# Optimization experiments

Hardware: AMD Instinct MI355X
Metric: run time of the kernel (lower is better)

The kernel has to match this reference:

```python
import jax, jax.numpy as jnp
import numpy as np

NT, C, B, N, H, E = 32768, 128, 64, 512, 4, 524288  # total nodes, channels, graphs, nodes/graph, heads, edges
DH = C // H
EPS = 1e-5


def batchnorm(x, g, b):
    # BatchNorm1d over the node dimension (training-mode batch statistics)
    m = x.mean(axis=0)
    v = x.var(axis=0)
    return (x - m) * jax.lax.rsqrt(v + EPS) * g + b


def setup_inputs() -> dict:
    key = jax.random.key(0)
    ks = jax.random.split(key, 8)
    s = 1.0 / np.sqrt(C)
    return dict(
        x=jax.random.normal(ks[0], (NT, C), jnp.float32),
        edge_index=jax.random.randint(ks[1], (2, E), 0, NT, dtype=jnp.int32),
        Wc=jax.random.normal(ks[2], (C, C), jnp.float32) * s,
        bc=jnp.zeros((C,), jnp.float32),
        in_proj_w=jax.random.normal(ks[3], (3 * C, C), jnp.float32) * s,
        in_proj_b=jnp.zeros((3 * C,), jnp.float32),
        out_proj_w=jax.random.normal(ks[4], (C, C), jnp.float32) * s,
        out_proj_b=jnp.zeros((C,), jnp.float32),
        gn1=jnp.ones((C,), jnp.float32), bn1=jnp.zeros((C,), jnp.float32),
        gn2=jnp.ones((C,), jnp.float32), bn2=jnp.zeros((C,), jnp.float32),
        gn3=jnp.ones((C,), jnp.float32), bn3=jnp.zeros((C,), jnp.float32),
        Wm1=jax.random.normal(ks[5], (2 * C, C), jnp.float32) * s,
        bm1=jnp.zeros((2 * C,), jnp.float32),
        Wm2=jax.random.normal(ks[6], (C, 2 * C), jnp.float32) / np.sqrt(2 * C),
        bm2=jnp.zeros((C,), jnp.float32),
    )


def reference(x, edge_index, Wc, bc, in_proj_w, in_proj_b, out_proj_w, out_proj_b,
              gn1, bn1, gn2, bn2, gn3, bn3, Wm1, bm1, Wm2, bm2):
    # --- local branch: mean-aggregation message passing + linear + residual + BN ---
    src, dst = edge_index[0], edge_index[1]
    agg = jax.ops.segment_sum(x[src], dst, num_segments=NT)            # [NT, C]
    cnt = jax.ops.segment_sum(jnp.ones((E, 1), x.dtype), dst, num_segments=NT)
    agg = agg / jnp.maximum(cnt, 1.0)
    h_local = agg @ Wc.T + bc + x                                       # dropout p=0 -> no-op
    h_local = batchnorm(h_local, gn1, bn1)

    # --- global branch: to_dense_batch (equal-size graphs -> reshape) + MHA ---
    hd = x.reshape(B, N, C)
    qkv = hd @ in_proj_w.T + in_proj_b                                  # [B, N, 3C]
    q, k, v = jnp.split(qkv, 3, axis=-1)
    q = q.reshape(B, N, H, DH).transpose(0, 2, 1, 3)                    # [B, H, N, DH]
    k = k.reshape(B, N, H, DH).transpose(0, 2, 1, 3)
    v = v.reshape(B, N, H, DH).transpose(0, 2, 1, 3)
    scores = jnp.einsum('bhqd,bhkd->bhqk', q, k) / np.sqrt(DH)          # [B, H, N, N]
    attn = jax.nn.softmax(scores, axis=-1)
    o = jnp.einsum('bhqk,bhkd->bhqd', attn, v)                          # [B, H, N, DH]
    o = o.transpose(0, 2, 1, 3).reshape(B, N, C)
    h_attn = (o @ out_proj_w.T + out_proj_b).reshape(NT, C) + x
    h_attn = batchnorm(h_attn, gn2, bn2)

    # --- combine + MLP + final norm ---
    out = h_local + h_attn
    out = out + (jax.nn.relu(out @ Wm1.T + bm1) @ Wm2.T + bm2)
    return batchnorm(out, gn3, bn3)
```

## Files before the change

kernel.cpp:

```cpp
#include <hip/hip_runtime.h>
#include <cstddef>

#define NT    32768
#define CCH   128
#define BB    64
#define NNODE 512
#define NHEAD 4
#define DHEAD 32
#define EE    524288
#define EPS   1e-5f
#define MAXDEG 96
#define SRCPAD 100
#define CURPAD 16
#define SSLOT  8

typedef unsigned short u16;
typedef unsigned int   u32;
typedef __attribute__((ext_vector_type(8))) short short8;
typedef __attribute__((ext_vector_type(4))) short short4v;
typedef __attribute__((ext_vector_type(4))) float f32x4;

__device__ __forceinline__ float b2f(u32 w) { return __uint_as_float(w << 16); }
__device__ __forceinline__ u16 f2b(float f) {
    u32 u = __float_as_uint(f);
    u += 0x7FFF + ((u >> 16) & 1);
    return (u16)(u >> 16);
}

__global__ __launch_bounds__(256) void prep_kernel(const float* __restrict__ x,
                                                   const float* __restrict__ Wc,
                                                   const float* __restrict__ Wqkv,
                                                   const float* __restrict__ Wo,
                                                   const float* __restrict__ Wm1,
                                                   const float* __restrict__ Wm2,
                                                   u16* __restrict__ xb,
                                                   u16* __restrict__ Wcb,
                                                   u16* __restrict__ Wqkvb,
                                                   u16* __restrict__ Wob,
                                                   u16* __restrict__ Wm1b,
                                                   u16* __restrict__ Wm2b,
                                                   const int* __restrict__ ei,
                                                   int* __restrict__ cursor,
                                                   int* __restrict__ bucket) {
    if (blockIdx.x >= 2120) {
        int e = (blockIdx.x - 2120) * 256 + threadIdx.x;
        int src = ei[e];
        int dst = ei[EE + e];
        int pos = atomicAdd(cursor + dst * CURPAD, 1);
        if (pos < MAXDEG) bucket[dst * MAXDEG + pos] = src;
        return;
    }
    int r = blockIdx.x * 256 + threadIdx.x;
    const float* src; u16* dst;
    if (r < 524288) { src = x; dst = xb; }
    else if ((r -= 524288) < 2048) { src = Wc; dst = Wcb; }
    else if ((r -= 2048) < 6144) { src = Wqkv; dst = Wqkvb; }
    else if ((r -= 6144) < 2048) { src = Wo; dst = Wob; }
    else if ((r -= 2048) < 4096) { src = Wm1; dst = Wm1b; }
    else { r -= 4096; src = Wm2; dst = Wm2b; }
    size_t base = (size_t)r * 8;
    float4 a = *(const float4*)(src + base);
    float4 b = *(const float4*)(src + base + 4);
    uint4 u;
    u.x = (u32)f2b(a.x) | ((u32)f2b(a.y) << 16);
    u.y = (u32)f2b(a.z) | ((u32)f2b(a.w) << 16);
    u.z = (u32)f2b(b.x) | ((u32)f2b(b.y) << 16);
    u.w = (u32)f2b(b.z) | ((u32)f2b(b.w) << 16);
    *(uint4*)(dst + base) = u;
}

__global__ __launch_bounds__(256) void aggregate(const int* __restrict__ bucket,
                                                 const int* __restrict__ cursor,
                                                 const u16* __restrict__ xb,
                                                 u16* __restrict__ agg) {
    __shared__ int srcs[16][SRCPAD];
    int ln = threadIdx.x >> 4;
    int c8 = threadIdx.x & 15;
    int n = blockIdx.x * 16 + ln;
    int d = min(cursor[n * CURPAD], MAXDEG);
    for (int j = c8; j < d; j += 16) srcs[ln][j] = bucket[n * MAXDEG + j];
    __syncthreads();
    float s0 = 0.f, s1 = 0.f, s2 = 0.f, s3 = 0.f;
    float s4 = 0.f, s5 = 0.f, s6 = 0.f, s7 = 0.f;
    const u16* xp = xb + c8 * 8;
    int j = 0;
    for (; j + 2 <= d; j += 2) {
        uint4 w0 = *(const uint4*)(xp + (size_t)srcs[ln][j] * CCH);
        uint4 w1 = *(const uint4*)(xp + (size_t)srcs[ln][j + 1] * CCH);
        s0 += b2f(w0.x & 0xffffu) + b2f(w1.x & 0xffffu);
        s1 += b2f(w0.x >> 16)     + b2f(w1.x >> 16);
        s2 += b2f(w0.y & 0xffffu) + b2f(w1.y & 0xffffu);
        s3 += b2f(w0.y >> 16)     + b2f(w1.y >> 16);
        s4 += b2f(w0.z & 0xffffu) + b2f(w1.z & 0xffffu);
        s5 += b2f(w0.z >> 16)     + b2f(w1.z >> 16);
        s6 += b2f(w0.w & 0xffffu) + b2f(w1.w & 0xffffu);
        s7 += b2f(w0.w >> 16)     + b2f(w1.w >> 16);
    }
    if (j < d) {
        uint4 w0 = *(const uint4*)(xp + (size_t)srcs[ln][j] * CCH);
        s0 += b2f(w0.x & 0xffffu);
        s1 += b2f(w0.x >> 16);
        s2 += b2f(w0.y & 0xffffu);
        s3 += b2f(w0.y >> 16);
        s4 += b2f(w0.z & 0xffffu);
        s5 += b2f(w0.z >> 16);
        s6 += b2f(w0.w & 0xffffu);
        s7 += b2f(w0.w >> 16);
    }
    float inv = 1.0f / fmaxf((float)d, 1.0f);
    uint4 out;
    out.x = (u32)f2b(s0 * inv) | ((u32)f2b(s1 * inv) << 16);
    out.y = (u32)f2b(s2 * inv) | ((u32)f2b(s3 * inv) << 16);
    out.z = (u32)f2b(s4 * inv) | ((u32)f2b(s5 * inv) << 16);
    out.w = (u32)f2b(s6 * inv) | ((u32)f2b(s7 * inv) << 16);
    *(uint4*)(agg + (size_t)n * CCH + c8 * 8) = out;
}

struct GemmSmem {
    u16 As[128 * 32];
    u16 Bs[128 * 32];
    u16 Cs[4][16 * 72];
    float csum[128];
    float csq[128];
};

template <bool RELU, int RESID, bool STATS>
__device__ __forceinline__ void gemm_body(GemmSmem& sm,
                                          const u16* __restrict__ A,
                                          const u16* __restrict__ W,
                                          const float* __restrict__ bias,
                                          const u16* __restrict__ residb,
                                          u16* __restrict__ outb, int ostride,
                                          float* __restrict__ sum, float* __restrict__ sumsq,
                                          int slotbase, int m0, int K) {
    int tid = threadIdx.x;
    int lane = tid & 63, wave = tid >> 6;
    int wm = (wave & 1) * 64, wn = (wave >> 1) * 64;
    int l15 = lane & 15, l4 = lane >> 4;

    if (STATS) {
        if (tid < 128) { sm.csum[tid] = 0.f; sm.csq[tid] = 0.f; }
    }

    f32x4 zero = {0.f, 0.f, 0.f, 0.f};
    f32x4 acc[4][4];
#pragma unroll
    for (int i = 0; i < 4; ++i)
#pragma unroll
        for (int j = 0; j < 4; ++j) acc[i][j] = zero;

    int srow = tid >> 2;
    int scol = (tid & 3) * 8;

    int kIter = K >> 5;
    uint4 a0 = *(const uint4*)(A + (size_t)(m0 + srow) * K + scol);
    uint4 a1 = *(const uint4*)(A + (size_t)(m0 + srow + 64) * K + scol);
    uint4 b0 = *(const uint4*)(W + (size_t)srow * K + scol);
    uint4 b1 = *(const uint4*)(W + (size_t)(srow + 64) * K + scol);
    for (int ki = 0; ki < kIter; ++ki) {
        if (ki) __syncthreads();
        *(uint4*)&sm.As[srow * 32 + scol] = a0;
        *(uint4*)&sm.As[(srow + 64) * 32 + scol] = a1;
        *(uint4*)&sm.Bs[srow * 32 + scol] = b0;
        *(uint4*)&sm.Bs[(srow + 64) * 32 + scol] = b1;
        if (ki + 1 < kIter) {
            int k0 = (ki + 1) * 32;
            a0 = *(const uint4*)(A + (size_t)(m0 + srow) * K + k0 + scol);
            a1 = *(const uint4*)(A + (size_t)(m0 + srow + 64) * K + k0 + scol);
            b0 = *(const uint4*)(W + (size_t)srow * K + k0 + scol);
            b1 = *(const uint4*)(W + (size_t)(srow + 64) * K + k0 + scol);
        }
        __syncthreads();
        short8 af[4], bf[4];
#pragma unroll
        for (int t = 0; t < 4; ++t) {
            af[t] = *(const short8*)&sm.As[(wm + t * 16 + l15) * 32 + l4 * 8];
            bf[t] = *(const short8*)&sm.Bs[(wn + t * 16 + l15) * 32 + l4 * 8];
        }
#pragma unroll
        for (int mt = 0; mt < 4; ++mt)
#pragma unroll
            for (int nt = 0; nt < 4; ++nt)
                acc[mt][nt] = __builtin_amdgcn_mfma_f32_16x16x32_bf16(af[mt], bf[nt], acc[mt][nt], 0, 0, 0);
    }

    float ps[4] = {0.f, 0.f, 0.f, 0.f};
    float pq[4] = {0.f, 0.f, 0.f, 0.f};
    int rl = lane >> 3;
    int cg = lane & 7;
#pragma unroll
    for (int mt = 0; mt < 4; ++mt) {
#pragma unroll
        for (int nt = 0; nt < 4; ++nt) {
            int lcol = wn + nt * 16 + l15;
            float bs = bias[lcol];
#pragma unroll
            for (int r = 0; r < 4; ++r) {
                int row = m0 + wm + mt * 16 + l4 * 4 + r;
                float v = acc[mt][nt][r] + bs;
                if (RESID == 2) v += b2f(residb[(size_t)row * 128 + lcol]);
                if (RELU) v = fmaxf(v, 0.0f);
                sm.Cs[wave][(l4 * 4 + r) * 72 + nt * 16 + l15] = f2b(v);
                if (STATS) { ps[nt] += v; pq[nt] += v * v; }
            }
        }
#pragma unroll
        for (int p = 0; p < 2; ++p) {
            int lrow = p * 8 + rl;
            uint4 wv = *(const uint4*)&sm.Cs[wave][lrow * 72 + cg * 8];
            int grow = m0 + wm + mt * 16 + lrow;
            *(uint4*)(outb + (size_t)grow * ostride + wn + cg * 8) = wv;
        }
    }
    if (STATS) {
#pragma unroll
        for (int nt = 0; nt < 4; ++nt) {
            atomicAdd(&sm.csum[wn + nt * 16 + l15], ps[nt]);
            atomicAdd(&sm.csq[wn + nt * 16 + l15], pq[nt]);
        }
        __syncthreads();
        if (tid < 128) {
            atomicAdd(sum + slotbase + tid, sm.csum[tid]);
            atomicAdd(sumsq + slotbase + tid, sm.csq[tid]);
        }
    }
}

__global__ __launch_bounds__(256) void gemm_wc_qkv(const u16* __restrict__ aggb,
                                                   const u16* __restrict__ Wcb,
                                                   const float* __restrict__ bc,
                                                   const u16* __restrict__ xb,
                                                   u16* __restrict__ hlocb,
                                                   float* __restrict__ sum1,
                                                   float* __restrict__ sq1,
                                                   const u16* __restrict__ Wqkvb,
                                                   const float* __restrict__ bqkv,
                                                   u16* __restrict__ qkvb) {
    __shared__ GemmSmem sm;
    int y = blockIdx.y;
    int m0 = blockIdx.x * 128;
    if (y == 0) {
        gemm_body<false, 2, true>(sm, aggb, Wcb, bc, xb, hlocb, 128, sum1, sq1,
                                  (blockIdx.x & (SSLOT - 1)) << 7, m0, 128);
    } else {
        gemm_body<false, 0, false>(sm, xb, Wqkvb + (size_t)(y - 1) * 16384,
                                   bqkv + (y - 1) * 128, nullptr,
                                   qkvb + (y - 1) * 128, 384, nullptr, nullptr, 0, m0, 128);
    }
}

__global__ __launch_bounds__(256) void gemm_wo(const u16* __restrict__ ob,
                                               const u16* __restrict__ Wob,
                                               const float* __restrict__ bo,
                                               const u16* __restrict__ xb,
                                               u16* __restrict__ t2b,
                                               float* __restrict__ sum2, float* __restrict__ sq2) {
    __shared__ GemmSmem sm;
    gemm_body<false, 2, true>(sm, ob, Wob, bo, xb, t2b, 128, sum2, sq2,
                              (blockIdx.x & (SSLOT - 1)) << 7, blockIdx.x * 128, 128);
}

__global__ __launch_bounds__(256) void gemm_mlp2(const u16* __restrict__ hidb,
                                                 const u16* __restrict__ Wm2b,
                                                 const float* __restrict__ bm2,
                                                 const u16* __restrict__ shb,
                                                 u16* __restrict__ out2b,
                                                 float* __restrict__ sum3, float* __restrict__ sq3) {
    __shared__ GemmSmem sm;
    gemm_body<false, 2, true>(sm, hidb, Wm2b, bm2, shb, out2b, 128, sum3, sq3,
                              (blockIdx.x & (SSLOT - 1)) << 7, blockIdx.x * 128, 256);
}

__global__ __launch_bounds__(256) void gemm_m1c(const u16* __restrict__ hlocb,
                                                const u16* __restrict__ t2b,
                                                const float* __restrict__ sum1,
                                                const float* __restrict__ sq1,
                                                const float* __restrict__ g1,
                                                const float* __restrict__ bt1,
                                                const float* __restrict__ sum2,
                                                const float* __restrict__ sq2,
                                                const float* __restrict__ g2,
                                                const float* __restrict__ bt2,
                                                u16* __restrict__ shb,
                                                const u16* __restrict__ Wm1b,
                                                const float* __restrict__ bm1,
                                                u16* __restrict__ hidb) {
    __shared__ u16 As[128 * 32];
    __shared__ u16 Bs[128 * 32];
    __shared__ u16 Cs[4][16 * 72];
    __shared__ float AF1[128], BF1[128], AF2[128], BF2[128];
    int tid = threadIdx.x;
    {
        int c = tid & 127;
        const float* sm = (tid < 128) ? sum1 : sum2;
        const float* sq = (tid < 128) ? sq1 : sq2;
        const float* g  = (tid < 128) ? g1 : g2;
        const float* bt = (tid < 128) ? bt1 : bt2;
        float s = 0.f, q = 0.f;
#pragma unroll
        for (int sl = 0; sl < SSLOT; ++sl) { s += sm[sl * 128 + c]; q += sq[sl * 128 + c]; }
        float m = s * (1.0f / NT);
        float v = q * (1.0f / NT) - m * m;
        float a = g[c] * rsqrtf(v + EPS);
        if (tid < 128) { AF1[c] = a; BF1[c] = bt[c] - m * a; }
        else           { AF2[c] = a; BF2[c] = bt[c] - m * a; }
    }
    int m0 = blockIdx.x * 128, n0 = blockIdx.y * 128;
    int lane = tid & 63, wave = tid >> 6;
    int wm = (wave & 1) * 64, wn = (wave >> 1) * 64;
    int l15 = lane & 15, l4 = lane >> 4;

    f32x4 zero = {0.f, 0.f, 0.f, 0.f};
    f32x4 acc[4][4];
#pragma unroll
    for (int i = 0; i < 4; ++i)
#pragma unroll
        for (int j = 0; j < 4; ++j) acc[i][j] = zero;

    int srow = tid >> 2;
    int scol = (tid & 3) * 8;
    bool wr = (blockIdx.y == 0);

    uint4 h0 = *(const uint4*)(hlocb + (size_t)(m0 + srow) * 128 + scol);
    uint4 h1 = *(const uint4*)(hlocb + (size_t)(m0 + srow + 64) * 128 + scol);
    uint4 t0 = *(const uint4*)(t2b + (size_t)(m0 + srow) * 128 + scol);
    uint4 t1 = *(const uint4*)(t2b + (size_t)(m0 + srow + 64) * 128 + scol);
    uint4 b0 = *(const uint4*)(Wm1b + (size_t)(n0 + srow) * 128 + scol);
    uint4 b1 = *(const uint4*)(Wm1b + (size_t)(n0 + srow + 64) * 128 + scol);
    __syncthreads();
    for (int ki = 0; ki < 4; ++ki) {
        int k0 = ki * 32;
        if (ki) __syncthreads();
        uint4 c0, c1;
        {
            const u32 hw[4] = {h0.x, h0.y, h0.z, h0.w};
            const u32 tw[4] = {t0.x, t0.y, t0.z, t0.w};
            u32 ow[4];
#pragma unroll
            for (int p = 0; p < 4; ++p) {
                int cc = k0 + scol + p * 2;
                float v0 = AF1[cc] * b2f(hw[p] & 0xffffu) + BF1[cc] + AF2[cc] * b2f(tw[p] & 0xffffu) + BF2[cc];
                float v1 = AF1[cc + 1] * b2f(hw[p] >> 16) + BF1[cc + 1] + AF2[cc + 1] * b2f(tw[p] >> 16) + BF2[cc + 1];
                ow[p] = (u32)f2b(v0) | ((u32)f2b(v1) << 16);
            }
            c0.x = ow[0]; c0.y = ow[1]; c0.z = ow[2]; c0.w = ow[3];
        }
        {
            const u32 hw[4] = {h1.x, h1.y, h1.z, h1.w};
            const u32 tw[4] = {t1.x, t1.y, t1.z, t1.w};
            u32 ow[4];
#pragma unroll
            for (int p = 0; p < 4; ++p) {
                int cc = k0 + scol + p * 2;
                float v0 = AF1[cc] * b2f(hw[p] & 0xffffu) + BF1[cc] + AF2[cc] * b2f(tw[p] & 0xffffu) + BF2[cc];
                float v1 = AF1[cc + 1] * b2f(hw[p] >> 16) + BF1[cc + 1] + AF2[cc + 1] * b2f(tw[p] >> 16) + BF2[cc + 1];
                ow[p] = (u32)f2b(v0) | ((u32)f2b(v1) << 16);
            }
            c1.x = ow[0]; c1.y = ow[1]; c1.z = ow[2]; c1.w = ow[3];
        }
        *(uint4*)&As[srow * 32 + scol] = c0;
        *(uint4*)&As[(srow + 64) * 32 + scol] = c1;
        *(uint4*)&Bs[srow * 32 + scol] = b0;
        *(uint4*)&Bs[(srow + 64) * 32 + scol] = b1;
        if (wr) {
            *(uint4*)(shb + (size_t)(m0 + srow) * 128 + k0 + scol) = c0;
            *(uint4*)(shb + (size_t)(m0 + srow + 64) * 128 + k0 + scol) = c1;
        }
        if (ki < 3) {
            int kn = k0 + 32;
            h0 = *(const uint4*)(hlocb + (size_t)(m0 + srow) * 128 + kn + scol);
            h1 = *(const uint4*)(hlocb + (size_t)(m0 + srow + 64) * 128 + kn + scol);
            t0 = *(const uint4*)(t2b + (size_t)(m0 + srow) * 128 + kn + scol);
            t1 = *(const uint4*)(t2b + (size_t)(m0 + srow + 64) * 128 + kn + scol);
            b0 = *(const uint4*)(Wm1b + (size_t)(n0 + srow) * 128 + kn + scol);
            b1 = *(const uint4*)(Wm1b + (size_t)(n0 + srow + 64) * 128 + kn + scol);
        }
        __syncthreads();
        short8 af[4], bf[4];
#pragma unroll
        for (int t = 0; t < 4; ++t) {
            af[t] = *(const short8*)&As[(wm + t * 16 + l15) * 32 + l4 * 8];
            bf[t] = *(const short8*)&Bs[(wn + t * 16 + l15) * 32 + l4 * 8];
        }
#pragma unroll
        for (int mt = 0; mt < 4; ++mt)
#pragma unroll
            for (int nt = 0; nt < 4; ++nt)
                acc[mt][nt] = __builtin_amdgcn_mfma_f32_16x16x32_bf16(af[mt], bf[nt], acc[mt][nt], 0, 0, 0);
    }

    int rl = lane >> 3;
    int cg = lane & 7;
#pragma unroll
    for (int mt = 0; mt < 4; ++mt) {
#pragma unroll
        for (int nt = 0; nt < 4; ++nt) {
            int col = n0 + wn + nt * 16 + l15;
            float bs = bm1[col];
#pragma unroll
            for (int r = 0; r < 4; ++r) {
                float v = fmaxf(acc[mt][nt][r] + bs, 0.0f);
                Cs[wave][(l4 * 4 + r) * 72 + nt * 16 + l15] = f2b(v);
            }
        }
#pragma unroll
        for (int p = 0; p < 2; ++p) {
            int lrow = p * 8 + rl;
            uint4 wv = *(const uint4*)&Cs[wave][lrow * 72 + cg * 8];
            int grow = m0 + wm + mt * 16 + lrow;
            *(uint4*)(hidb + (size_t)grow * 256 + n0 + wn + cg * 8) = wv;
        }
    }
}

__global__ __launch_bounds__(256) void final_bn(const u16* __restrict__ X,
                                                const float* __restrict__ sum3,
                                                const float* __restrict__ sq3,
                                                const float* __restrict__ g3,
                                                const float* __restrict__ bt3,
                                                float* __restrict__ outp) {
    __shared__ float A3[128], B3[128];
    int t = threadIdx.x;
    if (t < 128) {
        float s = 0.f, q = 0.f;
#pragma unroll
        for (int sl = 0; sl < SSLOT; ++sl) { s += sum3[sl * 128 + t]; q += sq3[sl * 128 + t]; }
        float m = s * (1.0f / NT);
        float v = q * (1.0f / NT) - m * m;
        float a = g3[t] * rsqrtf(v + EPS);
        A3[t] = a;
        B3[t] = bt3[t] - m * a;
    }
    __syncthreads();
    int i8 = blockIdx.x * 256 + t;
    size_t i = (size_t)i8 * 8;
    int c = (int)(i & (CCH - 1));
    uint4 u = *(const uint4*)(X + i);
    float x[8];
    x[0] = b2f(u.x & 0xffffu); x[1] = b2f(u.x >> 16);
    x[2] = b2f(u.y & 0xffffu); x[3] = b2f(u.y >> 16);
    x[4] = b2f(u.z & 0xffffu); x[5] = b2f(u.z >> 16);
    x[6] = b2f(u.w & 0xffffu); x[7] = b2f(u.w >> 16);
    float4 o0, o1;
    o0.x = A3[c + 0] * x[0] + B3[c + 0];
    o0.y = A3[c + 1] * x[1] + B3[c + 1];
    o0.z = A3[c + 2] * x[2] + B3[c + 2];
    o0.w = A3[c + 3] * x[3] + B3[c + 3];
    o1.x = A3[c + 4] * x[4] + B3[c + 4];
    o1.y = A3[c + 5] * x[5] + B3[c + 5];
    o1.z = A3[c + 6] * x[6] + B3[c + 6];
    o1.w = A3[c + 7] * x[7] + B3[c + 7];
    *(float4*)(outp + i) = o0;
    *(float4*)(outp + i + 4) = o1;
}

__global__ __launch_bounds__(512) void attn_mfma(const u16* __restrict__ qkv,
                                                 u16* __restrict__ o) {
    __shared__ __align__(16) u16 Ks[512 * 40];
    __shared__ __align__(16) u16 Vt[32 * 520];
    int bh = blockIdx.x;
    int b = bh >> 2, h = bh & 3;
    int tid = threadIdx.x;
    int lane = tid & 63, wave = tid >> 6;
    int quad = lane >> 4, l15 = lane & 15;
    const float scale = 0.1767766952966369f;

    const u16* kvbase = qkv + (size_t)b * 512 * 384 + 128 + h * 32;
    for (int idx = tid; idx < 2048; idx += 512) {
        int row = idx >> 2, c = idx & 3;
        *(uint4*)&Ks[row * 40 + c * 8] = *(const uint4*)(kvbase + (size_t)row * 384 + c * 8);
    }
    for (int idx = tid; idx < 2048; idx += 512) {
        int row = idx >> 2, c = idx & 3;
        uint4 u = *(const uint4*)(kvbase + 128 + (size_t)row * 384 + c * 8);
        u16 e[8];
        *(uint4*)e = u;
#pragma unroll
        for (int i = 0; i < 8; ++i) Vt[(c * 8 + i) * 520 + row] = e[i];
    }
    __syncthreads();

    f32x4 zero = {0.f, 0.f, 0.f, 0.f};
    for (int qt = 0; qt < 4; ++qt) {
        int qbase = wave * 64 + qt * 16;
        short8 qf = *(const short8*)(qkv + (size_t)(b * 512 + qbase + l15) * 384 + h * 32 + quad * 8);
        float lq = 0.f;
        f32x4 oa[2] = {zero, zero};

        for (int kv0 = 0; kv0 < 512; kv0 += 64) {
            f32x4 s[4];
#pragma unroll
            for (int t = 0; t < 4; ++t) {
                short8 kb = *(const short8*)&Ks[(kv0 + t * 16 + l15) * 40 + quad * 8];
                s[t] = __builtin_amdgcn_mfma_f32_16x16x32_bf16(kb, qf, zero, 0, 0, 0);
            }
            short8 pa[4];
#pragma unroll
            for (int t = 0; t < 4; ++t) {
                float p0 = __expf(s[t][0] * scale);
                float p1 = __expf(s[t][1] * scale);
                float p2 = __expf(s[t][2] * scale);
                float p3 = __expf(s[t][3] * scale);
                lq += (p0 + p1) + (p2 + p3);
                short8 a8 = {(short)f2b(p0), (short)f2b(p1), (short)f2b(p2), (short)f2b(p3), 0, 0, 0, 0};
                pa[t] = a8;
            }
#pragma unroll
            for (int t = 0; t < 4; ++t) {
                int tbase = kv0 + t * 16;
#pragma unroll
                for (int n = 0; n < 2; ++n) {
                    short4v v4 = *(const short4v*)&Vt[(n * 16 + l15) * 520 + tbase + quad * 4];
                    short8 vb = {v4.x, v4.y, v4.z, v4.w, 0, 0, 0, 0};
                    oa[n] = __builtin_amdgcn_mfma_f32_16x16x32_bf16(pa[t], vb, oa[n], 0, 0, 0);
                }
            }
        }
        lq += __shfl_xor(lq, 16);
        lq += __shfl_xor(lq, 32);
        u16* op = o + (size_t)(b * 512 + qbase) * 128 + h * 32;
#pragma unroll
        for (int r = 0; r < 4; ++r) {
            float Lr = __shfl(lq, quad * 4 + r);
            float inv = 1.0f / Lr;
#pragma unroll
            for (int n = 0; n < 2; ++n)
                op[(quad * 4 + r) * 128 + n * 16 + l15] = f2b(oa[n][r] * inv);
        }
    }
}

extern "C" void kernel_launch(void* const* d_in, const int* in_sizes, int n_in,
                              void* d_out, int out_size, void* d_ws, size_t ws_size,
                              hipStream_t stream) {
    const float* x    = (const float*)d_in[0];
    const int*   ei   = (const int*)d_in[1];
    const float* Wc   = (const float*)d_in[2];
    const float* bc   = (const float*)d_in[3];
    const float* Wqkv = (const float*)d_in[4];
    const float* bqkv = (const float*)d_in[5];
    const float* Wo   = (const float*)d_in[6];
    const float* bo   = (const float*)d_in[7];
    const float* gn1  = (const float*)d_in[8];
    const float* bn1b = (const float*)d_in[9];
    const float* gn2  = (const float*)d_in[10];
    const float* bn2b = (const float*)d_in[11];
    const float* gn3  = (const float*)d_in[12];
    const float* bn3b = (const float*)d_in[13];
    const float* Wm1  = (const float*)d_in[14];
    const float* bm1  = (const float*)d_in[15];
    const float* Wm2  = (const float*)d_in[16];
    const float* bm2  = (const float*)d_in[17];
    float* outp = (float*)d_out;

    char* w = (char*)d_ws;
    const size_t MB = 1024 * 1024;
    u16* xb    = (u16*)(w);
    u16* hlocb = (u16*)(w + 8 * MB);
    u16* t2b   = (u16*)(w + 16 * MB);
    u16* out2b = (u16*)(w + 24 * MB);
    u16* qkvb  = (u16*)(w + 32 * MB);
    u16* hidb  = (u16*)(w + 56 * MB);
    u16* shb   = (u16*)(w + 72 * MB);
    int* bucket = (int*)(w + 80 * MB);
    int* cursor = (int*)(w + 92 * MB);
    float* stats = (float*)(w + 94 * MB);
    u16* Wcb   = (u16*)(w + 95 * MB);
    u16* Wqkvb = Wcb + 16384;
    u16* Wob   = Wqkvb + 49152;
    u16* Wm1b  = Wob + 16384;
    u16* Wm2b  = Wm1b + 32768;
    u16* ob    = (u16*)(w + 96 * MB);
    float* sum1 = stats;                  float* sq1 = stats + 1024;
    float* sum2 = stats + 2048;           float* sq2 = stats + 3072;
    float* sum3 = stats + 4096;           float* sq3 = stats + 5120;

    hipMemsetAsync(cursor, 0, 2 * MB + 6 * 1024 * 4, stream);

    prep_kernel<<<2120 + 2048, 256, 0, stream>>>(x, Wc, Wqkv, Wo, Wm1, Wm2,
                                                 xb, Wcb, Wqkvb, Wob, Wm1b, Wm2b,
                                                 ei, cursor, bucket);

    aggregate<<<NT / 16, 256, 0, stream>>>(bucket, cursor, xb, shb);

    {
        dim3 g(NT / 128, 4);
        gemm_wc_qkv<<<g, 256, 0, stream>>>(shb, Wcb, bc, xb, hlocb, sum1, sq1,
                                           Wqkvb, bqkv, qkvb);
    }

    attn_mfma<<<BB * NHEAD, 512, 0, stream>>>(qkvb, ob);

    gemm_wo<<<NT / 128, 256, 0, stream>>>(ob, Wob, bo, xb, t2b, sum2, sq2);

    {
        dim3 g(NT / 128, 2);
        gemm_m1c<<<g, 256, 0, stream>>>(hlocb, t2b, sum1, sq1, gn1, bn1b,
                                        sum2, sq2, gn2, bn2b, shb, Wm1b, bm1, hidb);
    }

    gemm_mlp2<<<NT / 128, 256, 0, stream>>>(hidb, Wm2b, bm2, shb, out2b, sum3, sq3);

    final_bn<<<NT * CCH / 8 / 256, 256, 0, stream>>>(out2b, sum3, sq3, gn3, bn3b, outp);
}
```

Before: 252.6 us.

## Pack PV MFMA operands, shard edge bucketing by dst, widen aggregate threads

The attention PV step previously zero-padded half of each 16x16x32 MFMA operand. It now packs two 16-key tiles into one short8, halving the PV MFMA count. Edge bucketing now has each block scan a group of 2048 edges and handle only destinations with a given residue mod 8, which localizes atomics but reads the dst array eight times. The aggregate kernel now uses 32 lanes per node with 8-byte loads instead of 16 lanes with 16-byte loads, and drops the two-way unroll.

Result: faster. 246.0 us (-2.6%).

```diff
diff --git a/kernel.cpp b/kernel.cpp
--- a/kernel.cpp
+++ b/kernel.cpp
@@ -10,9 +10,9 @@
 #define EE    524288
 #define EPS   1e-5f
 #define MAXDEG 96
-#define SRCPAD 100
 #define CURPAD 16
 #define SSLOT  8
+#define EGRP  2048
 
 typedef unsigned short u16;
 typedef unsigned int   u32;
@@ -43,11 +43,18 @@
                                                    int* __restrict__ cursor,
                                                    int* __restrict__ bucket) {
     if (blockIdx.x >= 2120) {
-        int e = (blockIdx.x - 2120) * 256 + threadIdx.x;
-        int src = ei[e];
-        int dst = ei[EE + e];
-        int pos = atomicAdd(cursor + dst * CURPAD, 1);
-        if (pos < MAXDEG) bucket[dst * MAXDEG + pos] = src;
+        int b2 = blockIdx.x - 2120;
+        int k = b2 & 7;
+        int g = b2 >> 3;
+        int base_e = g * EGRP;
+        for (int j = threadIdx.x; j < EGRP; j += 256) {
+            int dst = ei[EE + base_e + j];
+            if ((dst & 7) == k) {
+                int src = ei[base_e + j];
+                int pos = atomicAdd(cursor + dst * CURPAD, 1);
+                if (pos < MAXDEG) bucket[dst * MAXDEG + pos] = src;
+            }
+        }
         return;
     }
     int r = blockIdx.x * 256 + threadIdx.x;
@@ -73,47 +80,26 @@
                                                  const int* __restrict__ cursor,
                                                  const u16* __restrict__ xb,
                                                  u16* __restrict__ agg) {
-    __shared__ int srcs[16][SRCPAD];
-    int ln = threadIdx.x >> 4;
-    int c8 = threadIdx.x & 15;
-    int n = blockIdx.x * 16 + ln;
+    int ln = threadIdx.x >> 5;
+    int c4 = threadIdx.x & 31;
+    int n = blockIdx.x * 8 + ln;
+    __shared__ int srcs[8][MAXDEG];
     int d = min(cursor[n * CURPAD], MAXDEG);
-    for (int j = c8; j < d; j += 16) srcs[ln][j] = bucket[n * MAXDEG + j];
+    for (int j = c4; j < d; j += 32) srcs[ln][j] = bucket[n * MAXDEG + j];
     __syncthreads();
     float s0 = 0.f, s1 = 0.f, s2 = 0.f, s3 = 0.f;
-    float s4 = 0.f, s5 = 0.f, s6 = 0.f, s7 = 0.f;
-    const u16* xp = xb + c8 * 8;
-    int j = 0;
-    for (; j + 2 <= d; j += 2) {
-        uint4 w0 = *(const uint4*)(xp + (size_t)srcs[ln][j] * CCH);
-        uint4 w1 = *(const uint4*)(xp + (size_t)srcs[ln][j + 1] * CCH);
-        s0 += b2f(w0.x & 0xffffu) + b2f(w1.x & 0xffffu);
-        s1 += b2f(w0.x >> 16)     + b2f(w1.x >> 16);
-        s2 += b2f(w0.y & 0xffffu) + b2f(w1.y & 0xffffu);
-        s3 += b2f(w0.y >> 16)     + b2f(w1.y >> 16);
-        s4 += b2f(w0.z & 0xffffu) + b2f(w1.z & 0xffffu);
-        s5 += b2f(w0.z >> 16)     + b2f(w1.z >> 16);
-        s6 += b2f(w0.w & 0xffffu) + b2f(w1.w & 0xffffu);
-        s7 += b2f(w0.w >> 16)     + b2f(w1.w >> 16);
-    }
-    if (j < d) {
-        uint4 w0 = *(const uint4*)(xp + (size_t)srcs[ln][j] * CCH);
-        s0 += b2f(w0.x & 0xffffu);
-        s1 += b2f(w0.x >> 16);
-        s2 += b2f(w0.y & 0xffffu);
-        s3 += b2f(w0.y >> 16);
-        s4 += b2f(w0.z & 0xffffu);
-        s5 += b2f(w0.z >> 16);
-        s6 += b2f(w0.w & 0xffffu);
-        s7 += b2f(w0.w >> 16);
+    for (int j = 0; j < d; ++j) {
+        uint2 w = *(const uint2*)(xb + (size_t)srcs[ln][j] * CCH + c4 * 4);
+        s0 += b2f(w.x & 0xffffu);
+        s1 += b2f(w.x >> 16);
+        s2 += b2f(w.y & 0xffffu);
+        s3 += b2f(w.y >> 16);
     }
     float inv = 1.0f / fmaxf((float)d, 1.0f);
-    uint4 out;
+    uint2 out;
     out.x = (u32)f2b(s0 * inv) | ((u32)f2b(s1 * inv) << 16);
     out.y = (u32)f2b(s2 * inv) | ((u32)f2b(s3 * inv) << 16);
-    out.z = (u32)f2b(s4 * inv) | ((u32)f2b(s5 * inv) << 16);
-    out.w = (u32)f2b(s6 * inv) | ((u32)f2b(s7 * inv) << 16);
-    *(uint4*)(agg + (size_t)n * CCH + c8 * 8) = out;
+    *(uint2*)(agg + (size_t)n * CCH + c4 * 4) = out;
 }
 
 struct GemmSmem {
@@ -494,7 +480,7 @@
                 short8 kb = *(const short8*)&Ks[(kv0 + t * 16 + l15) * 40 + quad * 8];
                 s[t] = __builtin_amdgcn_mfma_f32_16x16x32_bf16(kb, qf, zero, 0, 0, 0);
             }
-            short8 pa[4];
+            short8 pp[2];
 #pragma unroll
             for (int t = 0; t < 4; ++t) {
                 float p0 = __expf(s[t][0] * scale);
@@ -502,17 +488,22 @@
                 float p2 = __expf(s[t][2] * scale);
                 float p3 = __expf(s[t][3] * scale);
                 lq += (p0 + p1) + (p2 + p3);
-                short8 a8 = {(short)f2b(p0), (short)f2b(p1), (short)f2b(p2), (short)f2b(p3), 0, 0, 0, 0};
-                pa[t] = a8;
-            }
-#pragma unroll
-            for (int t = 0; t < 4; ++t) {
-                int tbase = kv0 + t * 16;
+                int hi = (t & 1) * 4;
+                pp[t >> 1][hi + 0] = (short)f2b(p0);
+                pp[t >> 1][hi + 1] = (short)f2b(p1);
+                pp[t >> 1][hi + 2] = (short)f2b(p2);
+                pp[t >> 1][hi + 3] = (short)f2b(p3);
+            }
+#pragma unroll
+            for (int tp = 0; tp < 2; ++tp) {
+                int tb = kv0 + tp * 32;
 #pragma unroll
                 for (int n = 0; n < 2; ++n) {
-                    short4v v4 = *(const short4v*)&Vt[(n * 16 + l15) * 520 + tbase + quad * 4];
-                    short8 vb = {v4.x, v4.y, v4.z, v4.w, 0, 0, 0, 0};
-                    oa[n] = __builtin_amdgcn_mfma_f32_16x16x32_bf16(pa[t], vb, oa[n], 0, 0, 0);
+                    const u16* vrow = &Vt[(n * 16 + l15) * 520 + tb + quad * 4];
+                    short4v va = *(const short4v*)vrow;
+                    short4v vb2 = *(const short4v*)(vrow + 16);
+                    short8 vv = {va.x, va.y, va.z, va.w, vb2.x, vb2.y, vb2.z, vb2.w};
+                    oa[n] = __builtin_amdgcn_mfma_f32_16x16x32_bf16(pp[tp], vv, oa[n], 0, 0, 0);
                 }
             }
         }
@@ -581,7 +572,7 @@
                                                  xb, Wcb, Wqkvb, Wob, Wm1b, Wm2b,
                                                  ei, cursor, bucket);
 
-    aggregate<<<NT / 16, 256, 0, stream>>>(bucket, cursor, xb, shb);
+    aggregate<<<NT / 8, 256, 0, stream>>>(bucket, cursor, xb, shb);
 
     {
         dim3 g(NT / 128, 4);
```
